# Optimization experiments

Measured on AMD Instinct MI355X. Metric: run time of the kernel, lower is better.

The kernel has to match this reference:

```python
import jax, jax.numpy as jnp
import numpy as np

B, S, N, H = 16, 512, 64, 768
E_TYPES, R_TYPES = 9, 10


def setup_inputs() -> dict:
    key = jax.random.key(0)
    ks = jax.random.split(key, 8)
    seq = jax.random.normal(ks[0], (B, S, H), dtype=jnp.float32)
    starts = jax.random.randint(ks[1], (B, N), 0, S - 16)
    lengths = jax.random.randint(ks[2], (B, N), 1, 16)
    entity_spans = jnp.stack([starts, starts + lengths], axis=-1).astype(jnp.int32)  # [B,N,2], start<end<=S
    attention_mask = jnp.ones((B, S), dtype=jnp.int32)
    sc = 0.02
    return {
        "sequence_output": seq,
        "attention_mask": attention_mask,
        "entity_spans": entity_spans,
        "W1e": jax.random.normal(ks[3], (H, H // 2), dtype=jnp.float32) * sc,
        "b1e": jnp.zeros((H // 2,), dtype=jnp.float32),
        "W2e": jax.random.normal(ks[4], (H // 2, E_TYPES), dtype=jnp.float32) * sc,
        "b2e": jnp.zeros((E_TYPES,), dtype=jnp.float32),
        "W1r": jax.random.normal(ks[5], (2 * H, H), dtype=jnp.float32) * sc,
        "b1r": jnp.zeros((H,), dtype=jnp.float32),
        "W2r": jax.random.normal(ks[6], (H, R_TYPES), dtype=jnp.float32) * sc,
        "b2r": jnp.zeros((R_TYPES,), dtype=jnp.float32),
    }


def reference(sequence_output, attention_mask, entity_spans,
              W1e, b1e, W2e, b2e, W1r, b1r, W2r, b2r):
    # Entity classifier over all tokens (dropout = identity in eval mode).
    # entity_logits: [B, S, E_TYPES]
    entity_logits = jax.nn.relu(sequence_output @ W1e + b1e) @ W2e + b2e

    # Span-mean entity representations, vectorized (replaces the Python
    # per-entity loop with .item() syncs). span mask: [B, N, S]
    pos = jnp.arange(S, dtype=entity_spans.dtype)
    start = entity_spans[..., 0:1]
    end = entity_spans[..., 1:2]
    span_mask = ((pos >= start) & (pos < end)).astype(sequence_output.dtype)
    counts = jnp.maximum(span_mask.sum(-1, keepdims=True), 1.0)
    # entity_repr: [B, N, H] = mean over tokens in each span
    entity_repr = jnp.einsum('bns,bsh->bnh', span_mask, sequence_output) / counts

    # Relation classification for all ordered pairs i<j (replaces nested
    # per-pair micro-launches with one batched GEMM).
    ii, jj = jnp.triu_indices(N, k=1)  # static, P = N*(N-1)/2
    pair_repr = jnp.concatenate([entity_repr[:, ii, :], entity_repr[:, jj, :]], axis=-1)  # [B,P,2H]
    relation_logits = jax.nn.relu(pair_repr @ W1r + b1r) @ W2r + b2r  # [B,P,R_TYPES]

    return entity_logits, entity_repr, relation_logits
```

## Files before the change

kernel.cpp:

```cpp
#include <hip/hip_runtime.h>
#include <hip/hip_bf16.h>


#define S_LEN 512
#define H_DIM 768
#define NPAIR 2016

typedef __bf16 bf16x8 __attribute__((ext_vector_type(8)));
typedef float f32x4 __attribute__((ext_vector_type(4)));

__device__ __forceinline__ void gload_lds16(const void* g, void* l) {
    __builtin_amdgcn_global_load_lds(
        (const __attribute__((address_space(1))) void*)g,
        (__attribute__((address_space(3))) void*)l, 16, 0, 0);
}

__device__ __forceinline__ ushort f2bf(float x) {
    __hip_bfloat16 h = __float2bfloat16(x);
    return *(ushort*)&h;
}

__global__ __launch_bounds__(256) void prep_all_k(
    const float* __restrict__ seq, const int* __restrict__ spans,
    const float* __restrict__ W1e, const float* __restrict__ W1r,
    const float* __restrict__ W2e, const float* __restrict__ W2r,
    const float* __restrict__ b2r,
    float* __restrict__ erep, ushort* __restrict__ erep_bf,
    ushort* __restrict__ W1et, ushort* __restrict__ W1rt,
    ushort* __restrict__ W2et, ushort* __restrict__ W2rt,
    int* __restrict__ ptab, float* __restrict__ rlog,
    ushort* __restrict__ seq_bf)
{
    __shared__ float t[32][33];
    const int bid = blockIdx.x, tid = threadIdx.x;

    if (bid < 1024) {
        const int bn = bid, b = bn >> 6;
        const int s0 = spans[bn * 2], s1 = spans[bn * 2 + 1];
        int lo = s0 < 0 ? 0 : s0;
        int hi = s1 > S_LEN ? S_LEN : s1;
        int cnt = hi - lo;
        if (cnt < 1) cnt = 1;
        const float inv = 1.f / (float)cnt;
        for (int c = tid; c < H_DIM; c += 256) {
            float acc = 0.f;
            for (int s = lo; s < hi; ++s)
                acc += seq[((size_t)b * S_LEN + s) * H_DIM + c];
            float v = acc * inv;
            erep[(size_t)bn * H_DIM + c] = v;
            erep_bf[(size_t)bn * H_DIM + c] = f2bf(v);
        }
    } else if (bid < 2464) {
        const float* src; ushort* dst; int b2, C;
        if (bid < 1312)      { b2 = bid - 1024; src = W1e; dst = W1et; C = 384; }
        else if (bid < 1888) { b2 = bid - 1312; src = W1r; dst = W1rt; C = 768; }
        else                 { b2 = bid - 1888; src = W1r + 768 * 768; dst = W1rt + 768 * 768; C = 768; }
        const int br = b2 % 24, bc = b2 / 24;
        const int r = tid >> 5, c = tid & 31;
        #pragma unroll
        for (int p = 0; p < 4; ++p) {
            int rr = r + p * 8;
            t[rr][c] = src[(size_t)(br * 32 + rr) * C + bc * 32 + c];
        }
        __syncthreads();
        #pragma unroll
        for (int p = 0; p < 4; ++p) {
            int rr = r + p * 8;
            dst[(size_t)(bc * 32 + rr) * 768 + br * 32 + c] = f2bf(t[c][rr]);
        }
    } else if (bid < 2552) {
        int idx = (bid - 2464) * 256 + tid;
        if (idx < 12288) {
            int col = idx / 768, k = idx % 768;
            W2rt[idx] = (col < 10) ? f2bf(W2r[k * 10 + col]) : (ushort)0;
        } else if (idx < 18432) {
            int u = idx - 12288;
            int col = u / 384, k = u % 384;
            W2et[u] = (col < 9) ? f2bf(W2e[k * 9 + col]) : (ushort)0;
        } else {
            int u = idx - 18432;
            int i = u >> 6, j = u & 63;
            if (j > i) {
                int p = i * 63 - i * (i - 1) / 2 + (j - i - 1);
                ptab[p] = (i << 8) | j;
            }
        }
    } else if (bid < 2680) {
        for (int n = (bid - 2552) * 256 + tid; n < 16 * NPAIR * 10; n += 128 * 256)
            rlog[n] = b2r[n % 10];
    } else {
        for (int i = (bid - 2680) * 256 + tid; i < (8192 * 768) / 4; i += 1024 * 256) {
            float4 v = ((const float4*)seq)[i];
            ushort4 o;
            o.x = f2bf(v.x); o.y = f2bf(v.y); o.z = f2bf(v.z); o.w = f2bf(v.w);
            ((ushort4*)seq_bf)[i] = o;
        }
    }
}

template<int MT, int EPI>
__global__ __launch_bounds__(256) void mfma_gemm_k(
    const ushort* __restrict__ A, const ushort* __restrict__ Bt,
    const float* __restrict__ bias, void* __restrict__ Cout,
    int M, int N, int K)
{
    constexpr int MI = MT / 32;
    __shared__ ushort As[MT * 32];
    __shared__ ushort Bs[4096];

    const int tid = threadIdx.x;
    const int lane = tid & 63, wid = tid >> 6;
    const int wr = wid >> 1, wc = wid & 1;
    const int m0 = blockIdx.y * MT, n0 = blockIdx.x * 128;
    const int fr = lane & 15, kg = lane >> 4;

    const int srow = tid >> 2, skq = (tid & 3) * 8;
    const ushort* ag0 = A + (size_t)(m0 + srow) * K + skq;
    const ushort* ag1 = A + (size_t)(m0 + 64 + srow) * K + skq;
    const ushort* bg0 = Bt + (size_t)(n0 + srow) * K + skq;
    const ushort* bg1 = Bt + (size_t)(n0 + 64 + srow) * K + skq;
    ushort* al0 = &As[tid * 8];
    ushort* al1 = &As[2048 + tid * 8];
    ushort* bl0 = &Bs[tid * 8];
    ushort* bl1 = &Bs[2048 + tid * 8];

    int aoff[MI], boff[4];
    #pragma unroll
    for (int i = 0; i < MI; ++i)
        aoff[i] = (wr * (MT / 2) + i * 16 + fr) * 32 + kg * 8;
    #pragma unroll
    for (int i = 0; i < 4; ++i)
        boff[i] = (wc * 64 + i * 16 + fr) * 32 + kg * 8;

    f32x4 acc[MI][4] = {};

    for (int k0 = 0; k0 < K; k0 += 32) {
        __syncthreads();
        gload_lds16(ag0 + k0, al0);
        if constexpr (MT == 128) gload_lds16(ag1 + k0, al1);
        gload_lds16(bg0 + k0, bl0);
        gload_lds16(bg1 + k0, bl1);
        __syncthreads();
        bf16x8 af[MI], bv[4];
        #pragma unroll
        for (int i = 0; i < MI; ++i) af[i] = *(const bf16x8*)&As[aoff[i]];
        #pragma unroll
        for (int i = 0; i < 4; ++i) bv[i] = *(const bf16x8*)&Bs[boff[i]];
        #pragma unroll
        for (int mi = 0; mi < MI; ++mi)
            #pragma unroll
            for (int nj = 0; nj < 4; ++nj)
                acc[mi][nj] = __builtin_amdgcn_mfma_f32_16x16x32_bf16(
                    af[mi], bv[nj], acc[mi][nj], 0, 0, 0);
    }

    if (EPI == 0) {
        __hip_bfloat16* Cb = (__hip_bfloat16*)Cout;
        float bcol[4];
        #pragma unroll
        for (int nj = 0; nj < 4; ++nj) bcol[nj] = bias[n0 + wc * 64 + nj * 16 + fr];
        #pragma unroll
        for (int mi = 0; mi < MI; ++mi)
            #pragma unroll
            for (int j = 0; j < 4; ++j) {
                size_t rb = (size_t)(m0 + wr * (MT / 2) + mi * 16 + kg * 4 + j) * N
                          + n0 + wc * 64 + fr;
                #pragma unroll
                for (int nj = 0; nj < 4; ++nj)
                    Cb[rb + nj * 16] = __float2bfloat16(
                        fmaxf(acc[mi][nj][j] + bcol[nj], 0.f));
            }
    } else {
        float* Cf = (float*)Cout;
        #pragma unroll
        for (int mi = 0; mi < MI; ++mi)
            #pragma unroll
            for (int j = 0; j < 4; ++j) {
                size_t rb = (size_t)(m0 + wr * (MT / 2) + mi * 16 + kg * 4 + j) * N
                          + n0 + wc * 64 + fr;
                #pragma unroll
                for (int nj = 0; nj < 4; ++nj)
                    Cf[rb + nj * 16] = acc[mi][nj][j];
            }
    }
}

__global__ __launch_bounds__(256) void elogmm_k(
    const ushort* __restrict__ H1, const ushort* __restrict__ W2et,
    const float* __restrict__ b2e, float* __restrict__ out)
{
    const int tid = threadIdx.x;
    const int lane = tid & 63, wid = tid >> 6;
    const int fr = lane & 15, kg = lane >> 4;
    const int rbase = blockIdx.x * 64 + wid * 16;

    f32x4 acc = {};
    #pragma unroll
    for (int c = 0; c < 12; ++c) {
        const int kk = c * 32 + kg * 8;
        bf16x8 av = *(const bf16x8*)(H1 + (size_t)(rbase + fr) * 384 + kk);
        bf16x8 bv = *(const bf16x8*)(W2et + fr * 384 + kk);
        acc = __builtin_amdgcn_mfma_f32_16x16x32_bf16(av, bv, acc, 0, 0, 0);
    }
    if (fr < 9) {
        const float bias = b2e[fr];
        #pragma unroll
        for (int j = 0; j < 4; ++j)
            out[(size_t)(rbase + kg * 4 + j) * 9 + fr] = acc[j] + bias;
    }
}

__global__ __launch_bounds__(256) void relmm_k(
    const float* __restrict__ UV,
    const float* __restrict__ b1r,
    const ushort* __restrict__ W2rt,
    const int* __restrict__ ptab,
    float* __restrict__ rlog)
{
    const int tid = threadIdx.x;
    const int lane = tid & 63, wid = tid >> 6;
    const int fr = lane & 15, kg = lane >> 4;
    const int pb = blockIdx.x % 126, kb = blockIdx.x / 126;
    const int p0 = pb * 256;

    size_t uoff[4], voff[4];
    #pragma unroll
    for (int q = 0; q < 4; ++q) {
        int p = p0 + wid * 64 + q * 16 + fr;
        unsigned bb = (unsigned)p / 2016u;
        unsigned pp = (unsigned)p - bb * 2016u;
        int ij = ptab[pp];
        uoff[q] = ((size_t)(bb * 64 + (ij >> 8))) * 1536;
        voff[q] = ((size_t)(bb * 64 + (ij & 255))) * 1536 + 768;
    }

    f32x4 acc[4] = {};

    for (int c = kb * 12; c < kb * 12 + 12; ++c) {
        const int k0 = c * 32, kk = k0 + kg * 8;
        const bf16x8 bv = *(const bf16x8*)(W2rt + fr * 768 + kk);
        const float4 bb0 = *(const float4*)(b1r + kk);
        const float4 bb1 = *(const float4*)(b1r + kk + 4);
        #pragma unroll
        for (int q = 0; q < 4; ++q) {
            float4 u0 = *(const float4*)(UV + uoff[q] + kk);
            float4 u1 = *(const float4*)(UV + uoff[q] + kk + 4);
            float4 v0 = *(const float4*)(UV + voff[q] + kk);
            float4 v1 = *(const float4*)(UV + voff[q] + kk + 4);
            ushort h[8];
            h[0] = f2bf(fmaxf(u0.x + v0.x + bb0.x, 0.f));
            h[1] = f2bf(fmaxf(u0.y + v0.y + bb0.y, 0.f));
            h[2] = f2bf(fmaxf(u0.z + v0.z + bb0.z, 0.f));
            h[3] = f2bf(fmaxf(u0.w + v0.w + bb0.w, 0.f));
            h[4] = f2bf(fmaxf(u1.x + v1.x + bb1.x, 0.f));
            h[5] = f2bf(fmaxf(u1.y + v1.y + bb1.y, 0.f));
            h[6] = f2bf(fmaxf(u1.z + v1.z + bb1.z, 0.f));
            h[7] = f2bf(fmaxf(u1.w + v1.w + bb1.w, 0.f));
            bf16x8 av = *(bf16x8*)h;
            acc[q] = __builtin_amdgcn_mfma_f32_16x16x32_bf16(av, bv, acc[q], 0, 0, 0);
        }
    }

    if (fr < 10) {
        #pragma unroll
        for (int q = 0; q < 4; ++q)
            #pragma unroll
            for (int j = 0; j < 4; ++j) {
                int p = p0 + wid * 64 + q * 16 + kg * 4 + j;
                atomicAdd(&rlog[(size_t)p * 10 + fr], acc[q][j]);
            }
    }
}

extern "C" void kernel_launch(void* const* d_in, const int* in_sizes, int n_in,
                              void* d_out, int out_size, void* d_ws, size_t ws_size,
                              hipStream_t stream)
{
    const float* seq   = (const float*)d_in[0];
    const int*   spans = (const int*)d_in[2];
    const float* W1e   = (const float*)d_in[3];
    const float* b1e   = (const float*)d_in[4];
    const float* W2e   = (const float*)d_in[5];
    const float* b2e   = (const float*)d_in[6];
    const float* W1r   = (const float*)d_in[7];
    const float* b1r   = (const float*)d_in[8];
    const float* W2r   = (const float*)d_in[9];
    const float* b2r   = (const float*)d_in[10];

    float* out  = (float*)d_out;
    float* elog = out;
    float* erep = out + 73728;
    float* rlog = out + 73728 + 786432;

    char* ws = (char*)d_ws;
    ushort* seq_bf  = (ushort*)ws;
    float*  UV      = (float*)ws;
    ushort* W1et    = (ushort*)(ws + 12582912);
    ushort* W1rt    = (ushort*)(ws + 13172736);
    ushort* erep_bf = (ushort*)(ws + 15532032);
    ushort* H1bf    = (ushort*)(ws + 17104896);
    ushort* W2rt    = (ushort*)(ws + 23396352);
    int*    ptab    = (int*)   (ws + 23420928);
    ushort* W2et    = (ushort*)(ws + 23428992);

    prep_all_k<<<3704, 256, 0, stream>>>(seq, spans, W1e, W1r, W2e, W2r, b2r,
                                         erep, erep_bf, W1et, W1rt, W2et, W2rt,
                                         ptab, rlog, seq_bf);
    mfma_gemm_k<64, 0><<<dim3(3, 128), 256, 0, stream>>>(
        seq_bf, W1et, b1e, H1bf, 8192, 384, 768);
    elogmm_k<<<128, 256, 0, stream>>>(H1bf, W2et, b2e, elog);
    mfma_gemm_k<64, 1><<<dim3(12, 16), 256, 0, stream>>>(
        erep_bf, W1rt, nullptr, UV, 1024, 1536, 768);
    relmm_k<<<252, 256, 0, stream>>>(UV, b1r, W2rt, ptab, rlog);
}
```

Before: 165.8 us.

## Double-buffer LDS tiles in MFMA GEMM and split relation K across more blocks

The MFMA GEMM now uses two LDS buffers and prefetches the next K tile with global_load_lds while running MFMAs on the current tile. This removes one barrier per iteration and hides global load latency. Separately, the relation kernel splits K into 3 chunks of 8 steps instead of 2 chunks of 12, launching 378 blocks instead of 252 for more parallelism. The cost is twice the LDS use per block and more atomic or partial-sum contributions to the relation logits.

```diff
diff --git a/kernel.cpp b/kernel.cpp
--- a/kernel.cpp
+++ b/kernel.cpp
@@ -105,8 +105,8 @@
     int M, int N, int K)
 {
     constexpr int MI = MT / 32;
-    __shared__ ushort As[MT * 32];
-    __shared__ ushort Bs[4096];
+    __shared__ ushort As[2][MT * 32];
+    __shared__ ushort Bs[2][4096];
 
     const int tid = threadIdx.x;
     const int lane = tid & 63, wid = tid >> 6;
@@ -119,10 +119,6 @@
     const ushort* ag1 = A + (size_t)(m0 + 64 + srow) * K + skq;
     const ushort* bg0 = Bt + (size_t)(n0 + srow) * K + skq;
     const ushort* bg1 = Bt + (size_t)(n0 + 64 + srow) * K + skq;
-    ushort* al0 = &As[tid * 8];
-    ushort* al1 = &As[2048 + tid * 8];
-    ushort* bl0 = &Bs[tid * 8];
-    ushort* bl1 = &Bs[2048 + tid * 8];
 
     int aoff[MI], boff[4];
     #pragma unroll
@@ -134,18 +130,43 @@
 
     f32x4 acc[MI][4] = {};
 
-    for (int k0 = 0; k0 < K; k0 += 32) {
+    const int nsteps = K / 32;
+
+    gload_lds16(ag0, &As[0][tid * 8]);
+    if constexpr (MT == 128) gload_lds16(ag1, &As[0][2048 + tid * 8]);
+    gload_lds16(bg0, &Bs[0][tid * 8]);
+    gload_lds16(bg1, &Bs[0][2048 + tid * 8]);
+    asm volatile("s_waitcnt vmcnt(0)");
+    __syncthreads();
+
+    int cur = 0;
+    for (int t = 0; t < nsteps - 1; ++t) {
+        const int kn = (t + 1) * 32;
+        gload_lds16(ag0 + kn, &As[cur ^ 1][tid * 8]);
+        if constexpr (MT == 128) gload_lds16(ag1 + kn, &As[cur ^ 1][2048 + tid * 8]);
+        gload_lds16(bg0 + kn, &Bs[cur ^ 1][tid * 8]);
+        gload_lds16(bg1 + kn, &Bs[cur ^ 1][2048 + tid * 8]);
+        bf16x8 af[MI], bv[4];
+        #pragma unroll
+        for (int i = 0; i < MI; ++i) af[i] = *(const bf16x8*)&As[cur][aoff[i]];
+        #pragma unroll
+        for (int i = 0; i < 4; ++i) bv[i] = *(const bf16x8*)&Bs[cur][boff[i]];
+        #pragma unroll
+        for (int mi = 0; mi < MI; ++mi)
+            #pragma unroll
+            for (int nj = 0; nj < 4; ++nj)
+                acc[mi][nj] = __builtin_amdgcn_mfma_f32_16x16x32_bf16(
+                    af[mi], bv[nj], acc[mi][nj], 0, 0, 0);
+        asm volatile("s_waitcnt vmcnt(0)");
         __syncthreads();
-        gload_lds16(ag0 + k0, al0);
-        if constexpr (MT == 128) gload_lds16(ag1 + k0, al1);
-        gload_lds16(bg0 + k0, bl0);
-        gload_lds16(bg1 + k0, bl1);
-        __syncthreads();
+        cur ^= 1;
+    }
+    {
         bf16x8 af[MI], bv[4];
         #pragma unroll
-        for (int i = 0; i < MI; ++i) af[i] = *(const bf16x8*)&As[aoff[i]];
-        #pragma unroll
-        for (int i = 0; i < 4; ++i) bv[i] = *(const bf16x8*)&Bs[boff[i]];
+        for (int i = 0; i < MI; ++i) af[i] = *(const bf16x8*)&As[cur][aoff[i]];
+        #pragma unroll
+        for (int i = 0; i < 4; ++i) bv[i] = *(const bf16x8*)&Bs[cur][boff[i]];
         #pragma unroll
         for (int mi = 0; mi < MI; ++mi)
             #pragma unroll
@@ -236,7 +257,7 @@
 
     f32x4 acc[4] = {};
 
-    for (int c = kb * 12; c < kb * 12 + 12; ++c) {
+    for (int c = kb * 8; c < kb * 8 + 8; ++c) {
         const int k0 = c * 32, kk = k0 + kg * 8;
         const bf16x8 bv = *(const bf16x8*)(W2rt + fr * 768 + kk);
         const float4 bb0 = *(const float4*)(b1r + kk);
@@ -311,5 +332,5 @@
     elogmm_k<<<128, 256, 0, stream>>>(H1bf, W2et, b2e, elog);
     mfma_gemm_k<64, 1><<<dim3(12, 16), 256, 0, stream>>>(
         erep_bf, W1rt, nullptr, UV, 1024, 1536, 768);
-    relmm_k<<<252, 256, 0, stream>>>(UV, b1r, W2rt, ptab, rlog);
-}
+    relmm_k<<<378, 256, 0, stream>>>(UV, b1r, W2rt, ptab, rlog);
+}
```

New measurement: 165.7 us. Within noise of the previous version (-0.1%).

## Merge GEMMs and post-kernels into shared launches with 4-stage LDS pipeline

Applied to the files above, without the earlier changes.

The two first-layer GEMMs are merged into one launch, and so are the two small second-layer kernels, cutting five launches to three. Each GEMM tile now uses a 4-buffer LDS ring fed by async global-to-LDS loads, waited on with explicit vmcnt, and takes one barrier per k-step instead of two. The relation kernel's K split goes from 2 to 3 chunks for more blocks, at the cost of more atomics. UV moves to its own workspace region so it no longer aliases seq_bf, which is required because both GEMMs now run concurrently.

```diff
diff --git a/kernel.cpp b/kernel.cpp
--- a/kernel.cpp
+++ b/kernel.cpp
@@ -98,56 +98,61 @@
     }
 }
 
-template<int MT, int EPI>
-__global__ __launch_bounds__(256) void mfma_gemm_k(
+template<int EPI>
+__device__ __forceinline__ void gemm_body(
     const ushort* __restrict__ A, const ushort* __restrict__ Bt,
     const float* __restrict__ bias, void* __restrict__ Cout,
-    int M, int N, int K)
-{
-    constexpr int MI = MT / 32;
-    __shared__ ushort As[MT * 32];
-    __shared__ ushort Bs[4096];
-
+    int bx, int by, int N, int K, ushort* As, ushort* Bs)
+{
     const int tid = threadIdx.x;
     const int lane = tid & 63, wid = tid >> 6;
     const int wr = wid >> 1, wc = wid & 1;
-    const int m0 = blockIdx.y * MT, n0 = blockIdx.x * 128;
+    const int m0 = by * 64, n0 = bx * 128;
     const int fr = lane & 15, kg = lane >> 4;
 
     const int srow = tid >> 2, skq = (tid & 3) * 8;
     const ushort* ag0 = A + (size_t)(m0 + srow) * K + skq;
-    const ushort* ag1 = A + (size_t)(m0 + 64 + srow) * K + skq;
     const ushort* bg0 = Bt + (size_t)(n0 + srow) * K + skq;
     const ushort* bg1 = Bt + (size_t)(n0 + 64 + srow) * K + skq;
-    ushort* al0 = &As[tid * 8];
-    ushort* al1 = &As[2048 + tid * 8];
-    ushort* bl0 = &Bs[tid * 8];
-    ushort* bl1 = &Bs[2048 + tid * 8];
-
-    int aoff[MI], boff[4];
+
+    int aoff[2], boff[4];
     #pragma unroll
-    for (int i = 0; i < MI; ++i)
-        aoff[i] = (wr * (MT / 2) + i * 16 + fr) * 32 + kg * 8;
+    for (int i = 0; i < 2; ++i)
+        aoff[i] = (wr * 32 + i * 16 + fr) * 32 + kg * 8;
     #pragma unroll
     for (int i = 0; i < 4; ++i)
         boff[i] = (wc * 64 + i * 16 + fr) * 32 + kg * 8;
 
-    f32x4 acc[MI][4] = {};
-
-    for (int k0 = 0; k0 < K; k0 += 32) {
-        __syncthreads();
-        gload_lds16(ag0 + k0, al0);
-        if constexpr (MT == 128) gload_lds16(ag1 + k0, al1);
-        gload_lds16(bg0 + k0, bl0);
-        gload_lds16(bg1 + k0, bl1);
-        __syncthreads();
-        bf16x8 af[MI], bv[4];
-        #pragma unroll
-        for (int i = 0; i < MI; ++i) af[i] = *(const bf16x8*)&As[aoff[i]];
-        #pragma unroll
-        for (int i = 0; i < 4; ++i) bv[i] = *(const bf16x8*)&Bs[boff[i]];
-        #pragma unroll
-        for (int mi = 0; mi < MI; ++mi)
+    const int nsteps = K / 32;
+
+    auto STAGE = [&](int kt, int buf) {
+        const int kn = kt * 32;
+        gload_lds16(ag0 + kn, As + buf * 2048 + tid * 8);
+        gload_lds16(bg0 + kn, Bs + buf * 4096 + tid * 8);
+        gload_lds16(bg1 + kn, Bs + buf * 4096 + 2048 + tid * 8);
+    };
+
+    STAGE(0, 0);
+    STAGE(1, 1);
+    STAGE(2, 2);
+
+    f32x4 acc[2][4] = {};
+
+    for (int t = 0; t < nsteps; ++t) {
+        if (t < nsteps - 2)       asm volatile("s_waitcnt vmcnt(6)" ::: "memory");
+        else if (t == nsteps - 2) asm volatile("s_waitcnt vmcnt(3)" ::: "memory");
+        else                      asm volatile("s_waitcnt vmcnt(0)" ::: "memory");
+        __builtin_amdgcn_s_barrier();
+        __builtin_amdgcn_sched_barrier(0);
+        if (t + 3 < nsteps) STAGE(t + 3, (t + 3) & 3);
+        const int buf = t & 3;
+        bf16x8 af[2], bv[4];
+        #pragma unroll
+        for (int i = 0; i < 2; ++i) af[i] = *(const bf16x8*)&As[buf * 2048 + aoff[i]];
+        #pragma unroll
+        for (int i = 0; i < 4; ++i) bv[i] = *(const bf16x8*)&Bs[buf * 4096 + boff[i]];
+        #pragma unroll
+        for (int mi = 0; mi < 2; ++mi)
             #pragma unroll
             for (int nj = 0; nj < 4; ++nj)
                 acc[mi][nj] = __builtin_amdgcn_mfma_f32_16x16x32_bf16(
@@ -160,10 +165,10 @@
         #pragma unroll
         for (int nj = 0; nj < 4; ++nj) bcol[nj] = bias[n0 + wc * 64 + nj * 16 + fr];
         #pragma unroll
-        for (int mi = 0; mi < MI; ++mi)
+        for (int mi = 0; mi < 2; ++mi)
             #pragma unroll
             for (int j = 0; j < 4; ++j) {
-                size_t rb = (size_t)(m0 + wr * (MT / 2) + mi * 16 + kg * 4 + j) * N
+                size_t rb = (size_t)(m0 + wr * 32 + mi * 16 + kg * 4 + j) * N
                           + n0 + wc * 64 + fr;
                 #pragma unroll
                 for (int nj = 0; nj < 4; ++nj)
@@ -173,10 +178,10 @@
     } else {
         float* Cf = (float*)Cout;
         #pragma unroll
-        for (int mi = 0; mi < MI; ++mi)
+        for (int mi = 0; mi < 2; ++mi)
             #pragma unroll
             for (int j = 0; j < 4; ++j) {
-                size_t rb = (size_t)(m0 + wr * (MT / 2) + mi * 16 + kg * 4 + j) * N
+                size_t rb = (size_t)(m0 + wr * 32 + mi * 16 + kg * 4 + j) * N
                           + n0 + wc * 64 + fr;
                 #pragma unroll
                 for (int nj = 0; nj < 4; ++nj)
@@ -185,90 +190,102 @@
     }
 }
 
-__global__ __launch_bounds__(256) void elogmm_k(
+__global__ __launch_bounds__(256) void gemm2_k(
+    const ushort* __restrict__ seq_bf, const ushort* __restrict__ W1et,
+    const float* __restrict__ b1e, ushort* __restrict__ H1bf,
+    const ushort* __restrict__ erep_bf, const ushort* __restrict__ W1rt,
+    float* __restrict__ UV)
+{
+    __shared__ ushort As[4 * 2048];
+    __shared__ ushort Bs[4 * 4096];
+    const int bid = blockIdx.x;
+    if (bid < 384) {
+        gemm_body<0>(seq_bf, W1et, b1e, H1bf, bid % 3, bid / 3, 384, 768, As, Bs);
+    } else {
+        const int b2 = bid - 384;
+        gemm_body<1>(erep_bf, W1rt, nullptr, UV, b2 % 12, b2 / 12, 1536, 768, As, Bs);
+    }
+}
+
+__global__ __launch_bounds__(256) void post_k(
+    const float* __restrict__ UV, const float* __restrict__ b1r,
+    const ushort* __restrict__ W2rt, const int* __restrict__ ptab,
+    float* __restrict__ rlog,
     const ushort* __restrict__ H1, const ushort* __restrict__ W2et,
-    const float* __restrict__ b2e, float* __restrict__ out)
+    const float* __restrict__ b2e, float* __restrict__ elog)
 {
     const int tid = threadIdx.x;
     const int lane = tid & 63, wid = tid >> 6;
     const int fr = lane & 15, kg = lane >> 4;
-    const int rbase = blockIdx.x * 64 + wid * 16;
-
-    f32x4 acc = {};
-    #pragma unroll
-    for (int c = 0; c < 12; ++c) {
-        const int kk = c * 32 + kg * 8;
-        bf16x8 av = *(const bf16x8*)(H1 + (size_t)(rbase + fr) * 384 + kk);
-        bf16x8 bv = *(const bf16x8*)(W2et + fr * 384 + kk);
-        acc = __builtin_amdgcn_mfma_f32_16x16x32_bf16(av, bv, acc, 0, 0, 0);
-    }
-    if (fr < 9) {
-        const float bias = b2e[fr];
-        #pragma unroll
-        for (int j = 0; j < 4; ++j)
-            out[(size_t)(rbase + kg * 4 + j) * 9 + fr] = acc[j] + bias;
-    }
-}
-
-__global__ __launch_bounds__(256) void relmm_k(
-    const float* __restrict__ UV,
-    const float* __restrict__ b1r,
-    const ushort* __restrict__ W2rt,
-    const int* __restrict__ ptab,
-    float* __restrict__ rlog)
-{
-    const int tid = threadIdx.x;
-    const int lane = tid & 63, wid = tid >> 6;
-    const int fr = lane & 15, kg = lane >> 4;
-    const int pb = blockIdx.x % 126, kb = blockIdx.x / 126;
-    const int p0 = pb * 256;
-
-    size_t uoff[4], voff[4];
-    #pragma unroll
-    for (int q = 0; q < 4; ++q) {
-        int p = p0 + wid * 64 + q * 16 + fr;
-        unsigned bb = (unsigned)p / 2016u;
-        unsigned pp = (unsigned)p - bb * 2016u;
-        int ij = ptab[pp];
-        uoff[q] = ((size_t)(bb * 64 + (ij >> 8))) * 1536;
-        voff[q] = ((size_t)(bb * 64 + (ij & 255))) * 1536 + 768;
-    }
-
-    f32x4 acc[4] = {};
-
-    for (int c = kb * 12; c < kb * 12 + 12; ++c) {
-        const int k0 = c * 32, kk = k0 + kg * 8;
-        const bf16x8 bv = *(const bf16x8*)(W2rt + fr * 768 + kk);
-        const float4 bb0 = *(const float4*)(b1r + kk);
-        const float4 bb1 = *(const float4*)(b1r + kk + 4);
+    const int bid = blockIdx.x;
+
+    if (bid < 378) {
+        const int pb = bid % 126, kb = bid / 126;
+        const int p0 = pb * 256;
+
+        size_t uoff[4], voff[4];
         #pragma unroll
         for (int q = 0; q < 4; ++q) {
-            float4 u0 = *(const float4*)(UV + uoff[q] + kk);
-            float4 u1 = *(const float4*)(UV + uoff[q] + kk + 4);
-            float4 v0 = *(const float4*)(UV + voff[q] + kk);
-            float4 v1 = *(const float4*)(UV + voff[q] + kk + 4);
-            ushort h[8];
-            h[0] = f2bf(fmaxf(u0.x + v0.x + bb0.x, 0.f));
-            h[1] = f2bf(fmaxf(u0.y + v0.y + bb0.y, 0.f));
-            h[2] = f2bf(fmaxf(u0.z + v0.z + bb0.z, 0.f));
-            h[3] = f2bf(fmaxf(u0.w + v0.w + bb0.w, 0.f));
-            h[4] = f2bf(fmaxf(u1.x + v1.x + bb1.x, 0.f));
-            h[5] = f2bf(fmaxf(u1.y + v1.y + bb1.y, 0.f));
-            h[6] = f2bf(fmaxf(u1.z + v1.z + bb1.z, 0.f));
-            h[7] = f2bf(fmaxf(u1.w + v1.w + bb1.w, 0.f));
-            bf16x8 av = *(bf16x8*)h;
-            acc[q] = __builtin_amdgcn_mfma_f32_16x16x32_bf16(av, bv, acc[q], 0, 0, 0);
-        }
-    }
-
-    if (fr < 10) {
-        #pragma unroll
-        for (int q = 0; q < 4; ++q)
-            #pragma unroll
-            for (int j = 0; j < 4; ++j) {
-                int p = p0 + wid * 64 + q * 16 + kg * 4 + j;
-                atomicAdd(&rlog[(size_t)p * 10 + fr], acc[q][j]);
+            int p = p0 + wid * 64 + q * 16 + fr;
+            unsigned bb = (unsigned)p / 2016u;
+            unsigned pp = (unsigned)p - bb * 2016u;
+            int ij = ptab[pp];
+            uoff[q] = ((size_t)(bb * 64 + (ij >> 8))) * 1536;
+            voff[q] = ((size_t)(bb * 64 + (ij & 255))) * 1536 + 768;
+        }
+
+        f32x4 acc[4] = {};
+
+        for (int c = kb * 8; c < kb * 8 + 8; ++c) {
+            const int k0 = c * 32, kk = k0 + kg * 8;
+            const bf16x8 bv = *(const bf16x8*)(W2rt + fr * 768 + kk);
+            const float4 bb0 = *(const float4*)(b1r + kk);
+            const float4 bb1 = *(const float4*)(b1r + kk + 4);
+            #pragma unroll
+            for (int q = 0; q < 4; ++q) {
+                float4 u0 = *(const float4*)(UV + uoff[q] + kk);
+                float4 u1 = *(const float4*)(UV + uoff[q] + kk + 4);
+                float4 v0 = *(const float4*)(UV + voff[q] + kk);
+                float4 v1 = *(const float4*)(UV + voff[q] + kk + 4);
+                ushort h[8];
+                h[0] = f2bf(fmaxf(u0.x + v0.x + bb0.x, 0.f));
+                h[1] = f2bf(fmaxf(u0.y + v0.y + bb0.y, 0.f));
+                h[2] = f2bf(fmaxf(u0.z + v0.z + bb0.z, 0.f));
+                h[3] = f2bf(fmaxf(u0.w + v0.w + bb0.w, 0.f));
+                h[4] = f2bf(fmaxf(u1.x + v1.x + bb1.x, 0.f));
+                h[5] = f2bf(fmaxf(u1.y + v1.y + bb1.y, 0.f));
+                h[6] = f2bf(fmaxf(u1.z + v1.z + bb1.z, 0.f));
+                h[7] = f2bf(fmaxf(u1.w + v1.w + bb1.w, 0.f));
+                bf16x8 av = *(bf16x8*)h;
+                acc[q] = __builtin_amdgcn_mfma_f32_16x16x32_bf16(av, bv, acc[q], 0, 0, 0);
             }
+        }
+
+        if (fr < 10) {
+            #pragma unroll
+            for (int q = 0; q < 4; ++q)
+                #pragma unroll
+                for (int j = 0; j < 4; ++j) {
+                    int p = p0 + wid * 64 + q * 16 + kg * 4 + j;
+                    atomicAdd(&rlog[(size_t)p * 10 + fr], acc[q][j]);
+                }
+        }
+    } else {
+        const int rbase = (bid - 378) * 64 + wid * 16;
+        f32x4 acc = {};
+        #pragma unroll
+        for (int c = 0; c < 12; ++c) {
+            const int kk = c * 32 + kg * 8;
+            bf16x8 av = *(const bf16x8*)(H1 + (size_t)(rbase + fr) * 384 + kk);
+            bf16x8 bv = *(const bf16x8*)(W2et + fr * 384 + kk);
+            acc = __builtin_amdgcn_mfma_f32_16x16x32_bf16(av, bv, acc, 0, 0, 0);
+        }
+        if (fr < 9) {
+            const float bias = b2e[fr];
+            #pragma unroll
+            for (int j = 0; j < 4; ++j)
+                elog[(size_t)(rbase + kg * 4 + j) * 9 + fr] = acc[j] + bias;
+        }
     }
 }
 
@@ -294,7 +311,6 @@
 
     char* ws = (char*)d_ws;
     ushort* seq_bf  = (ushort*)ws;
-    float*  UV      = (float*)ws;
     ushort* W1et    = (ushort*)(ws + 12582912);
     ushort* W1rt    = (ushort*)(ws + 13172736);
     ushort* erep_bf = (ushort*)(ws + 15532032);
@@ -302,14 +318,12 @@
     ushort* W2rt    = (ushort*)(ws + 23396352);
     int*    ptab    = (int*)   (ws + 23420928);
     ushort* W2et    = (ushort*)(ws + 23428992);
+    float*  UV      = (float*) (ws + 23441280);
 
     prep_all_k<<<3704, 256, 0, stream>>>(seq, spans, W1e, W1r, W2e, W2r, b2r,
                                          erep, erep_bf, W1et, W1rt, W2et, W2rt,
                                          ptab, rlog, seq_bf);
-    mfma_gemm_k<64, 0><<<dim3(3, 128), 256, 0, stream>>>(
-        seq_bf, W1et, b1e, H1bf, 8192, 384, 768);
-    elogmm_k<<<128, 256, 0, stream>>>(H1bf, W2et, b2e, elog);
-    mfma_gemm_k<64, 1><<<dim3(12, 16), 256, 0, stream>>>(
-        erep_bf, W1rt, nullptr, UV, 1024, 1536, 768);
-    relmm_k<<<252, 256, 0, stream>>>(UV, b1r, W2rt, ptab, rlog);
-}
+    gemm2_k<<<576, 256, 0, stream>>>(seq_bf, W1et, b1e, H1bf, erep_bf, W1rt, UV);
+    post_k<<<506, 256, 0, stream>>>(UV, b1r, W2rt, ptab, rlog,
+                                    H1bf, W2et, b2e, elog);
+}
```

New measurement: 150.4 us. 9.3% less time.
